# Kernel tuning notes

Measured on AMD Instinct MI355X. Metric: run time of the kernel, lower is better.

## Reference

```python
import jax, jax.numpy as jnp
import numpy as np

BATCH, SEQ, NUM_SUB, CB_SIZE, SUB_DIM = 8, 2048, 16, 1024, 64
EMB_DIM = NUM_SUB * SUB_DIM  # 1024


def setup_inputs() -> dict:
    key = jax.random.key(0)
    k1, k2 = jax.random.split(key)
    embeddings = jax.random.normal(k1, (BATCH, SEQ, EMB_DIM), dtype=jnp.float32)
    # stacked PQ codebooks: [num_subspaces, codebook_size, subspace_dim]
    codebooks = jax.random.normal(k2, (NUM_SUB, CB_SIZE, SUB_DIM), dtype=jnp.float32)
    return {"embeddings": embeddings, "codebooks": codebooks}


def reference(embeddings, codebooks):
    B, S, D = embeddings.shape
    M, K, d = codebooks.shape
    # [N, M, d] tokens split into subspaces
    x = embeddings.reshape(-1, M, d)
    x2 = jnp.sum(x * x, axis=-1, keepdims=True)            # [N, M, 1]
    c2 = jnp.sum(codebooks * codebooks, axis=-1)           # [M, K]
    xc = jnp.einsum('nmd,mkd->nmk', x, codebooks)          # [N, M, K]
    dist2 = x2 - 2.0 * xc + c2[None, :, :]
    indices = jnp.argmin(dist2, axis=-1)                   # [N, M] (argmin of sqdist == argmin of cdist)
    # gather nearest codeword per subspace: [N, M, d]
    quantized = jnp.take_along_axis(
        codebooks[None, :, :, :],                          # [1, M, K, d]
        indices[:, :, None, None],                         # [N, M, 1, 1]
        axis=2,
    )[:, :, 0, :]
    quantized = quantized.reshape(B, S, D)
    indices = indices.reshape(B, S, M).astype(jnp.int64)
    return quantized, indices
```

## Files before the change

### kernel.cpp

```cpp
#include <hip/hip_runtime.h>
#include <hip/hip_bf16.h>

#pragma clang fp contract(off)

#define NSUB 16
#define CBK  1024
#define SDIM 64
#define EMB  1024
#define NTOK 16384
#define TOKB 128
#define MARGIN 5e-3f

typedef __attribute__((ext_vector_type(8))) short bf16x8;
typedef __attribute__((ext_vector_type(4))) float f32x4;

__device__ __forceinline__ float fmul(float a, float b) { return __fmul_rn(a, b); }
__device__ __forceinline__ float fadd(float a, float b) { return __fadd_rn(a, b); }
__device__ __forceinline__ float fsub(float a, float b) { return __fsub_rn(a, b); }

__device__ __forceinline__ float np_sq64(const float* v) {
    float r[8];
    #pragma unroll
    for (int j = 0; j < 8; ++j) r[j] = fmul(v[j], v[j]);
    #pragma unroll
    for (int b = 1; b < 8; ++b) {
        #pragma unroll
        for (int j = 0; j < 8; ++j)
            r[j] = fadd(r[j], fmul(v[b * 8 + j], v[b * 8 + j]));
    }
    return fadd(fadd(fadd(r[0], r[1]), fadd(r[2], r[3])),
                fadd(fadd(r[4], r[5]), fadd(r[6], r[7])));
}

__device__ __forceinline__ void split_bf16(float v, short& hi, short& lo) {
    __hip_bfloat16 h = __float2bfloat16(v);
    float hf = __bfloat162float(h);
    __hip_bfloat16 e = __float2bfloat16(__fsub_rn(v, hf));
    hi = *(short*)&h;
    lo = *(short*)&e;
}

typedef const __attribute__((address_space(1))) unsigned int gu32;
typedef __attribute__((address_space(3))) unsigned int lu32;
__device__ __forceinline__ void stage16(const void* g, void* l) {
    __builtin_amdgcn_global_load_lds((gu32*)g, (lu32*)l, 16, 0, 0);
}

__global__ __launch_bounds__(256)
void prep_kernel(const float* __restrict__ cb,
                 unsigned short* __restrict__ bpack,
                 float* __restrict__ c2g)
{
    const int bx = blockIdx.x;
    const int m  = blockIdx.y;
    const int t  = threadIdx.x;
    const int w  = t >> 6, l = t & 63;
    const int tc = bx * 2 + (w & 1);
    const int c  = w >> 1;
    const int cw = tc * 16 + (l & 15);
    const int dq = (l >> 4) * 8;

    {
        const float* src = cb + ((size_t)m * CBK + cw) * SDIM + c * 32 + dq;
        bf16x8 hv, lv;
        #pragma unroll
        for (int j = 0; j < 8; ++j) {
            short h, e; split_bf16(-2.0f * src[j], h, e);
            hv[j] = h; lv[j] = e;
        }
        size_t base = (((size_t)(m * 64 + tc) * 2 + c) * 2) * 512 + (size_t)l * 8;
        *(bf16x8*)(bpack + base)       = hv;
        *(bf16x8*)(bpack + base + 512) = lv;
    }
    if (t < 32) {
        const int row = bx * 32 + t;
        c2g[m * CBK + row] = np_sq64(cb + ((size_t)m * CBK + row) * SDIM);
    }
}

__global__ __launch_bounds__(256)
void idx_transpose_kernel(const float* __restrict__ iws,
                          float* __restrict__ iout)
{
    const int tok = blockIdx.x * 256 + threadIdx.x;
    float v[NSUB];
    #pragma unroll
    for (int m = 0; m < NSUB; ++m)
        v[m] = iws[(size_t)m * NTOK + tok];
    float* dst = iout + (size_t)tok * NSUB;
    #pragma unroll
    for (int c = 0; c < 4; ++c)
        *(f32x4*)(dst + c * 4) = *(f32x4*)(v + c * 4);
}

__global__ __launch_bounds__(256, 4)
void pq_mfma_kernel(const float* __restrict__ emb,
                    const float* __restrict__ cb,
                    const unsigned short* __restrict__ bpack,
                    const float* __restrict__ c2g,
                    float* __restrict__ qout,
                    float* __restrict__ iws)
{
    __shared__ __align__(16) unsigned short bs[2][4 * 2048];
    __shared__ float C2s[CBK];
    __shared__ float red_v[256];
    __shared__ int   red_k[256];
    __shared__ int   bestk_s[TOKB];
    __shared__ int   flag_s[TOKB];
    __shared__ int   cnt_s;

    const int rank = blockIdx.x;
    const int m    = rank & 15;
    const int tok0 = (rank >> 4) * TOKB;

    const int t = threadIdx.x, w = t >> 6, l = t & 63;
    const int ln15 = l & 15, q = l >> 4;

    if (t == 0) cnt_s = 0;
    *(f32x4*)(C2s + t * 4) = *(const f32x4*)(c2g + m * CBK + t * 4);

    const unsigned short* gB = bpack + (size_t)m * 64 * 2048;

    {
        const unsigned short* src = gB + t * 8;
        #pragma unroll
        for (int j = 0; j < 4; ++j)
            stage16(src + j * 2048, &bs[0][j * 2048 + t * 8]);
    }

    bf16x8 xh[2][2], xl[2][2];
    #pragma unroll
    for (int r = 0; r < 2; ++r) {
        const int tok = tok0 + w * 32 + r * 16 + ln15;
        #pragma unroll
        for (int c = 0; c < 2; ++c) {
            const float* src = emb + (size_t)tok * EMB + m * SDIM + c * 32 + q * 8;
            float4 v0 = *(const float4*)(src);
            float4 v1 = *(const float4*)(src + 4);
            float vv[8] = {v0.x,v0.y,v0.z,v0.w,v1.x,v1.y,v1.z,v1.w};
            #pragma unroll
            for (int j = 0; j < 8; ++j) {
                short h, e; split_bf16(vv[j], h, e);
                xh[r][c][j] = h; xl[r][c][j] = e;
            }
        }
    }

    float v1t[2][4], v2t[2][4]; int k1t[2][4];
    #pragma unroll
    for (int r = 0; r < 2; ++r)
        #pragma unroll
        for (int g = 0; g < 4; ++g) { v1t[r][g] = 3.4e38f; v2t[r][g] = 3.4e38f; k1t[r][g] = 0; }

    __syncthreads();

#define COMPUTE_TILE(B0, B1, B2, B3, TC)                                        \
    {                                                                           \
        const int kk = (TC) * 16 + ln15;                                        \
        const float c2v = C2s[kk];                                              \
        _Pragma("unroll")                                                       \
        for (int r = 0; r < 2; ++r) {                                           \
            f32x4 acc = {c2v, c2v, c2v, c2v};                                   \
            acc = __builtin_amdgcn_mfma_f32_16x16x32_bf16(xh[r][0], B0, acc, 0, 0, 0); \
            acc = __builtin_amdgcn_mfma_f32_16x16x32_bf16(xh[r][1], B2, acc, 0, 0, 0); \
            acc = __builtin_amdgcn_mfma_f32_16x16x32_bf16(xl[r][0], B0, acc, 0, 0, 0); \
            acc = __builtin_amdgcn_mfma_f32_16x16x32_bf16(xl[r][1], B2, acc, 0, 0, 0); \
            acc = __builtin_amdgcn_mfma_f32_16x16x32_bf16(xh[r][0], B1, acc, 0, 0, 0); \
            acc = __builtin_amdgcn_mfma_f32_16x16x32_bf16(xh[r][1], B3, acc, 0, 0, 0); \
            _Pragma("unroll")                                                   \
            for (int g = 0; g < 4; ++g) {                                       \
                float s = acc[g];                                               \
                v2t[r][g] = fminf(v2t[r][g], fmaxf(s, v1t[r][g]));              \
                bool lt = s < v1t[r][g];                                        \
                v1t[r][g] = lt ? s : v1t[r][g];                                 \
                k1t[r][g] = lt ? kk : k1t[r][g];                                \
            }                                                                   \
        }                                                                       \
    }

    for (int ph = 0; ph < 16; ++ph) {
        const int buf = ph & 1;
        if (ph < 15) {
            const unsigned short* src = gB + (size_t)(ph + 1) * 8192 + t * 8;
            #pragma unroll
            for (int j = 0; j < 4; ++j)
                stage16(src + j * 2048, &bs[buf ^ 1][j * 2048 + t * 8]);
        }
        #pragma unroll
        for (int j = 0; j < 4; ++j) {
            const int tc = ph * 4 + j;
            const unsigned short* bp = &bs[buf][j * 2048 + l * 8];
            bf16x8 B0 = *(const bf16x8*)(bp);
            bf16x8 B1 = *(const bf16x8*)(bp + 512);
            bf16x8 B2 = *(const bf16x8*)(bp + 1024);
            bf16x8 B3 = *(const bf16x8*)(bp + 1536);
            COMPUTE_TILE(B0, B1, B2, B3, tc)
        }
        __syncthreads();
    }
#undef COMPUTE_TILE

    #pragma unroll
    for (int r = 0; r < 2; ++r) {
        #pragma unroll
        for (int g = 0; g < 4; ++g) {
            float v1 = v1t[r][g], v2 = v2t[r][g]; int k1 = k1t[r][g];
            #pragma unroll
            for (int mask = 1; mask < 16; mask <<= 1) {
                float ov1 = __shfl_xor(v1, mask);
                float ov2 = __shfl_xor(v2, mask);
                int   ok1 = __shfl_xor(k1, mask);
                if (ov1 < v1 || (ov1 == v1 && ok1 < k1)) {
                    v2 = fminf(v1, ov2);
                    v1 = ov1; k1 = ok1;
                } else {
                    v2 = fminf(v2, ov1);
                }
            }
            if (ln15 == 0) {
                const int token = w * 32 + r * 16 + q * 4 + g;
                if (v2 - v1 <= MARGIN) {
                    int slot = atomicAdd(&cnt_s, 1);
                    flag_s[slot] = token;
                } else {
                    bestk_s[token] = k1;
                    iws[(size_t)m * NTOK + tok0 + token] = (float)k1;
                }
            }
        }
    }
    __syncthreads();

    const int nflag = cnt_s;
    for (int f = 0; f < nflag; ++f) {
        const int token = flag_s[f];
        const float* xrow = emb + (size_t)(tok0 + token) * EMB + m * SDIM;
        const float x2v = np_sq64(xrow);
        float bs_ = 3.4e38f; int bk = CBK;
        #pragma unroll
        for (int rr = 0; rr < 4; ++rr) {
            const int k = t + 256 * rr;
            const float* crow = cb + ((size_t)m * CBK + k) * SDIM;
            float acc = 0.f;
            #pragma unroll
            for (int i = 0; i < 16; ++i) {
                float4 c4 = *(const float4*)(crow + 4 * i);
                float4 x4 = *(const float4*)(xrow + 4 * i);
                acc = __fmaf_rn(x4.x, c4.x, acc);
                acc = __fmaf_rn(x4.y, c4.y, acc);
                acc = __fmaf_rn(x4.z, c4.z, acc);
                acc = __fmaf_rn(x4.w, c4.w, acc);
            }
            const float dist = fadd(fsub(x2v, fmul(2.f, acc)), C2s[k]);
            if (dist < bs_) { bs_ = dist; bk = k; }
        }
        red_v[t] = bs_; red_k[t] = bk;
        __syncthreads();
        for (int off = 128; off > 0; off >>= 1) {
            if (t < off) {
                float o = red_v[t + off]; int ok = red_k[t + off];
                if (o < red_v[t] || (o == red_v[t] && ok < red_k[t])) {
                    red_v[t] = o; red_k[t] = ok;
                }
            }
            __syncthreads();
        }
        if (t == 0) {
            bestk_s[token] = red_k[0];
            iws[(size_t)m * NTOK + tok0 + token] = (float)red_k[0];
        }
        __syncthreads();
    }

    {
        const int tok = t >> 1, d0 = (t & 1) * 32;
        const int bk  = bestk_s[tok];
        const float* src = cb + ((size_t)m * CBK + bk) * SDIM + d0;
        float* dst = qout + (size_t)(tok0 + tok) * EMB + m * SDIM + d0;
        #pragma unroll
        for (int i = 0; i < 8; ++i)
            *(float4*)(dst + 4 * i) = *(const float4*)(src + 4 * i);
    }
}

extern "C" void kernel_launch(void* const* d_in, const int* in_sizes, int n_in,
                              void* d_out, int out_size, void* d_ws, size_t ws_size,
                              hipStream_t stream) {
    const float* emb = (const float*)d_in[0];
    const float* cb  = (const float*)d_in[1];
    float* qout = (float*)d_out;
    float* iout = (float*)d_out + (size_t)NTOK * EMB;

    unsigned short* bpack = (unsigned short*)d_ws;
    float* c2g = (float*)((char*)d_ws + 4u * 1024u * 1024u);
    float* iws = (float*)((char*)d_ws + 4u * 1024u * 1024u + 64u * 1024u);

    prep_kernel<<<dim3(32, 16), 256, 0, stream>>>(cb, bpack, c2g);
    pq_mfma_kernel<<<dim3(NTOK / TOKB * NSUB), 256, 0, stream>>>(
        emb, cb, bpack, c2g, qout, iws);
    idx_transpose_kernel<<<dim3(NTOK / 256), 256, 0, stream>>>(iws, iout);
}
```

Measured before the change: 283.0 us.

## Rescore flagged tokens with MFMA prefilter and candidate-only exact FP32 check

The fallback for tokens whose top-two distances fall within the margin is replaced. Instead of a full 1024-codeword FP32 scan per flagged token with block-wide reductions and syncs, each wave takes 16 flagged tokens and rescreens them with split-bf16 MFMA. It records a bitmask of candidate codeword columns within the margin and computes exact FP32 distances only for those candidates, finishing with a wave-shuffle argmin. This removes per-token __syncthreads and most of the redundant FP32 work, at the cost of a more complex path whose correctness depends on the candidate margin.

```diff
diff --git a/kernel.cpp b/kernel.cpp
--- a/kernel.cpp
+++ b/kernel.cpp
@@ -103,8 +103,6 @@
 {
     __shared__ __align__(16) unsigned short bs[2][4 * 2048];
     __shared__ float C2s[CBK];
-    __shared__ float red_v[256];
-    __shared__ int   red_k[256];
     __shared__ int   bestk_s[TOKB];
     __shared__ int   flag_s[TOKB];
     __shared__ int   cnt_s;
@@ -232,45 +230,100 @@
     __syncthreads();
 
     const int nflag = cnt_s;
-    for (int f = 0; f < nflag; ++f) {
-        const int token = flag_s[f];
-        const float* xrow = emb + (size_t)(tok0 + token) * EMB + m * SDIM;
-        const float x2v = np_sq64(xrow);
-        float bs_ = 3.4e38f; int bk = CBK;
-        #pragma unroll
-        for (int rr = 0; rr < 4; ++rr) {
-            const int k = t + 256 * rr;
-            const float* crow = cb + ((size_t)m * CBK + k) * SDIM;
-            float acc = 0.f;
-            #pragma unroll
-            for (int i = 0; i < 16; ++i) {
-                float4 c4 = *(const float4*)(crow + 4 * i);
-                float4 x4 = *(const float4*)(xrow + 4 * i);
-                acc = __fmaf_rn(x4.x, c4.x, acc);
-                acc = __fmaf_rn(x4.y, c4.y, acc);
-                acc = __fmaf_rn(x4.z, c4.z, acc);
-                acc = __fmaf_rn(x4.w, c4.w, acc);
-            }
-            const float dist = fadd(fsub(x2v, fmul(2.f, acc)), C2s[k]);
-            if (dist < bs_) { bs_ = dist; bk = k; }
-        }
-        red_v[t] = bs_; red_k[t] = bk;
-        __syncthreads();
-        for (int off = 128; off > 0; off >>= 1) {
-            if (t < off) {
-                float o = red_v[t + off]; int ok = red_k[t + off];
-                if (o < red_v[t] || (o == red_v[t] && ok < red_k[t])) {
-                    red_v[t] = o; red_k[t] = ok;
-                }
-            }
-            __syncthreads();
-        }
-        if (t == 0) {
-            bestk_s[token] = red_k[0];
-            iws[(size_t)m * NTOK + tok0 + token] = (float)red_k[0];
-        }
-        __syncthreads();
-    }
+    for (int g0 = w * 16; g0 < nflag; g0 += 64) {
+        const int slotL = g0 + ln15;
+        const int tokL  = flag_s[slotL < nflag ? slotL : g0];
+        bf16x8 fxh[2], fxl[2];
+        #pragma unroll
+        for (int c = 0; c < 2; ++c) {
+            const float* src = emb + (size_t)(tok0 + tokL) * EMB + m * SDIM + c * 32 + q * 8;
+            float4 v0 = *(const float4*)(src);
+            float4 v1 = *(const float4*)(src + 4);
+            float vv[8] = {v0.x,v0.y,v0.z,v0.w,v1.x,v1.y,v1.z,v1.w};
+            #pragma unroll
+            for (int j = 0; j < 8; ++j) {
+                short h, e; split_bf16(vv[j], h, e);
+                fxh[c][j] = h; fxl[c][j] = e;
+            }
+        }
+
+        unsigned long long cmask[4] = {0ull, 0ull, 0ull, 0ull};
+        float v1r[4] = {3.4e38f, 3.4e38f, 3.4e38f, 3.4e38f};
+        const unsigned short* bp0 = gB + (size_t)l * 8;
+        bf16x8 Bc0 = *(const bf16x8*)(bp0);
+        bf16x8 Bc1 = *(const bf16x8*)(bp0 + 512);
+        bf16x8 Bc2 = *(const bf16x8*)(bp0 + 1024);
+        bf16x8 Bc3 = *(const bf16x8*)(bp0 + 1536);
+        #pragma unroll 2
+        for (int tc = 0; tc < 64; ++tc) {
+            bf16x8 Bn0, Bn1, Bn2, Bn3;
+            if (tc < 63) {
+                const unsigned short* bpn = gB + (size_t)(tc + 1) * 2048 + (size_t)l * 8;
+                Bn0 = *(const bf16x8*)(bpn);
+                Bn1 = *(const bf16x8*)(bpn + 512);
+                Bn2 = *(const bf16x8*)(bpn + 1024);
+                Bn3 = *(const bf16x8*)(bpn + 1536);
+            }
+            const int kk = tc * 16 + ln15;
+            const float c2v = C2s[kk];
+            f32x4 acc = {c2v, c2v, c2v, c2v};
+            acc = __builtin_amdgcn_mfma_f32_16x16x32_bf16(fxh[0], Bc0, acc, 0, 0, 0);
+            acc = __builtin_amdgcn_mfma_f32_16x16x32_bf16(fxh[1], Bc2, acc, 0, 0, 0);
+            acc = __builtin_amdgcn_mfma_f32_16x16x32_bf16(fxl[0], Bc0, acc, 0, 0, 0);
+            acc = __builtin_amdgcn_mfma_f32_16x16x32_bf16(fxl[1], Bc2, acc, 0, 0, 0);
+            acc = __builtin_amdgcn_mfma_f32_16x16x32_bf16(fxh[0], Bc1, acc, 0, 0, 0);
+            acc = __builtin_amdgcn_mfma_f32_16x16x32_bf16(fxh[1], Bc3, acc, 0, 0, 0);
+            #pragma unroll
+            for (int g = 0; g < 4; ++g) {
+                float s = acc[g];
+                bool cand = (s <= v1r[g] + MARGIN);
+                cmask[g] |= cand ? (1ull << tc) : 0ull;
+                v1r[g] = fminf(v1r[g], s);
+            }
+            Bc0 = Bn0; Bc1 = Bn1; Bc2 = Bn2; Bc3 = Bn3;
+        }
+
+        #pragma unroll
+        for (int g = 0; g < 4; ++g) {
+            const int slot = g0 + q * 4 + g;
+            if (slot < nflag) {
+                const int token = flag_s[slot];
+                const float* xrow = emb + (size_t)(tok0 + token) * EMB + m * SDIM;
+                unsigned long long msk = cmask[g];
+                const float x2v = np_sq64(xrow);
+                float bv = 3.4e38f; int bk = CBK;
+                while (msk) {
+                    const int tc = __builtin_ctzll(msk);
+                    msk &= msk - 1;
+                    const int k = tc * 16 + ln15;
+                    const float* crow = cb + ((size_t)m * CBK + k) * SDIM;
+                    float acc = 0.f;
+                    #pragma unroll
+                    for (int i = 0; i < 16; ++i) {
+                        float4 c4 = *(const float4*)(crow + 4 * i);
+                        float4 x4 = *(const float4*)(xrow + 4 * i);
+                        acc = __fmaf_rn(x4.x, c4.x, acc);
+                        acc = __fmaf_rn(x4.y, c4.y, acc);
+                        acc = __fmaf_rn(x4.z, c4.z, acc);
+                        acc = __fmaf_rn(x4.w, c4.w, acc);
+                    }
+                    const float dist = fadd(fsub(x2v, fmul(2.f, acc)), C2s[k]);
+                    if (dist < bv) { bv = dist; bk = k; }
+                }
+                #pragma unroll
+                for (int mask = 1; mask < 16; mask <<= 1) {
+                    float ov = __shfl_xor(bv, mask);
+                    int   ok = __shfl_xor(bk, mask);
+                    if (ov < bv || (ov == bv && ok < bk)) { bv = ov; bk = ok; }
+                }
+                if (ln15 == 0) {
+                    bestk_s[token] = bk;
+                    iws[(size_t)m * NTOK + tok0 + token] = (float)bk;
+                }
+            }
+        }
+    }
+    __syncthreads();
 
     {
         const int tok = t >> 1, d0 = (t & 1) * 32;
```

Measured after the change: 253.8 us. 10.3% less time.
